# Kernel tuning notes

Hardware: AMD Instinct MI355X
Metric: run time of the kernel (lower is better)

## Reference

```python
import jax, jax.numpy as jnp
import numpy as np
import math

B, S, E = 2, 2048, 2048
H, KVH = 16, 4
HD = E // H  # 128
ROPE_BASE = 10000.0


def _rope_cos_sin(seq_len, dim, base=ROPE_BASE):
    inv_freq = 1.0 / (base ** (jnp.arange(0, dim, 2, dtype=jnp.float32) / dim))
    t = jnp.arange(seq_len, dtype=jnp.float32)
    freqs = jnp.outer(t, inv_freq)            # [S, dim/2]
    emb = jnp.concatenate([freqs, freqs], -1)  # [S, dim]
    return jnp.cos(emb), jnp.sin(emb)          # each [S, dim]


def _rotate_half(x):
    h = x.shape[-1] // 2
    return jnp.concatenate([-x[..., h:], x[..., :h]], axis=-1)


def setup_inputs() -> dict:
    key = jax.random.key(0)
    ks = jax.random.split(key, 6)
    x = jax.random.normal(ks[0], (B, S, E), dtype=jnp.float32)
    # xavier_uniform for Linear(in, out): weight stored as [out, in] in torch;
    # we store transposed [in, out] for x @ W.
    def xavier(k, fan_in, fan_out):
        a = math.sqrt(6.0 / (fan_in + fan_out))
        return jax.random.uniform(k, (fan_in, fan_out), jnp.float32, -a, a)
    wq = xavier(ks[1], E, H * HD)
    wk = xavier(ks[2], E, KVH * HD)
    wv = xavier(ks[3], E, KVH * HD)
    wo = xavier(ks[4], E, E)
    # causal mask: True above diagonal => masked
    attn_mask = jnp.triu(jnp.ones((S, S), dtype=bool), k=1)
    return {"x": x, "wq": wq, "wk": wk, "wv": wv, "wo": wo, "attn_mask": attn_mask}


def reference(x, wq, wk, wv, wo, attn_mask):
    b, s, _ = x.shape
    q = (x @ wq).reshape(b, s, H, HD).transpose(0, 2, 1, 3)     # [B,H,S,HD]
    k = (x @ wk).reshape(b, s, KVH, HD).transpose(0, 2, 1, 3)   # [B,KVH,S,HD]
    v = (x @ wv).reshape(b, s, KVH, HD).transpose(0, 2, 1, 3)
    cos, sin = _rope_cos_sin(s, HD)
    cos = cos[None, None]  # [1,1,S,HD]
    sin = sin[None, None]
    q = q * cos + _rotate_half(q) * sin
    k = k * cos + _rotate_half(k) * sin
    # repeat KV heads to match Q heads (GQA)
    groups = H // KVH
    k = jnp.repeat(k, groups, axis=1)  # [B,H,S,HD]
    v = jnp.repeat(v, groups, axis=1)
    scale = 1.0 / math.sqrt(HD)
    scores = jnp.einsum('bhqd,bhkd->bhqk', q, k) * scale  # [B,H,S,S]
    scores = jnp.where(attn_mask[None, None], -jnp.inf, scores)
    attn = jax.nn.softmax(scores, axis=-1)
    out = jnp.einsum('bhqk,bhkd->bhqd', attn, v)  # [B,H,S,HD]
    out = out.transpose(0, 2, 1, 3).reshape(b, s, E)
    return out @ wo
```

## Files before the change

### kernel.cpp

```cpp
#include <hip/hip_runtime.h>
#include <math.h>

#define S_LEN 2048
#define EDIM  2048
#define HDIM  128

typedef __attribute__((ext_vector_type(8))) __bf16 bf16x8;
typedef __attribute__((ext_vector_type(4))) __bf16 bf16x4;
typedef __attribute__((ext_vector_type(4))) float  f32x4;

__device__ __forceinline__ f32x4 mfma16x16x32(bf16x8 a, bf16x8 b, f32x4 c) {
  return __builtin_amdgcn_mfma_f32_16x16x32_bf16(a, b, c, 0, 0, 0);
}

__device__ __forceinline__ void gload_lds16(const __bf16* g, __bf16* l) {
  __builtin_amdgcn_global_load_lds(
      (const __attribute__((address_space(1))) void*)g,
      (__attribute__((address_space(3))) void*)l, 16, 0, 0);
}

__global__ void zero_flag(int* f) { *f = 0; }

__global__ void probe_dtype(const unsigned int* __restrict__ x, int* __restrict__ flag) {
  const int tid = threadIdx.x;
  int cnt = 0;
  for (int i = tid; i < 4096; i += 256) {
    unsigned e = (x[i] >> 7) & 0xFFu;
    cnt += (e >= 110u && e <= 135u) ? 1 : 0;
  }
  #pragma unroll
  for (int m = 1; m < 64; m <<= 1) cnt += __shfl_xor(cnt, m, 64);
  if ((tid & 63) == 0) atomicAdd(flag, cnt);
}

__global__ __launch_bounds__(256) void xconv(const void* __restrict__ xv,
                                             __bf16* __restrict__ xb,
                                             const int* __restrict__ flag) {
  const bool bf = (*flag > 2048);
  const size_t base = ((size_t)blockIdx.x * 256 + threadIdx.x) * 8;
  bf16x8 v;
  if (bf) {
    v = *(const bf16x8*)((const __bf16*)xv + base);
  } else {
    const float* xf = (const float*)xv + base;
    float4 f0 = *(const float4*)(xf);
    float4 f1 = *(const float4*)(xf + 4);
    v[0] = (__bf16)f0.x; v[1] = (__bf16)f0.y; v[2] = (__bf16)f0.z; v[3] = (__bf16)f0.w;
    v[4] = (__bf16)f1.x; v[5] = (__bf16)f1.y; v[6] = (__bf16)f1.z; v[7] = (__bf16)f1.w;
  }
  *(bf16x8*)(xb + base) = v;
}

__global__ __launch_bounds__(256) void trans_w(const void* __restrict__ Wv,
                                               __bf16* __restrict__ WT,
                                               int Kd, int Nd,
                                               const int* __restrict__ flag) {
  const bool bf = (*flag > 2048);
  __shared__ __bf16 t[64 * 72];
  const int tid = threadIdx.x;
  const int n0 = blockIdx.x * 64, k0 = blockIdx.y * 64;
  #pragma unroll
  for (int it = 0; it < 2; ++it) {
    int q = tid + it * 256;
    int r = q >> 3, c8 = q & 7;
    size_t gb = (size_t)(k0 + r) * Nd + n0 + c8 * 8;
    bf16x8 v;
    if (bf) {
      v = *(const bf16x8*)((const __bf16*)Wv + gb);
    } else {
      const float* wf = (const float*)Wv + gb;
      float4 f0 = *(const float4*)(wf);
      float4 f1 = *(const float4*)(wf + 4);
      v[0] = (__bf16)f0.x; v[1] = (__bf16)f0.y; v[2] = (__bf16)f0.z; v[3] = (__bf16)f0.w;
      v[4] = (__bf16)f1.x; v[5] = (__bf16)f1.y; v[6] = (__bf16)f1.z; v[7] = (__bf16)f1.w;
    }
    int eo = (c8 * 8) ^ (((r >> 3) & 7) * 8);
    *(bf16x8*)&t[r * 72 + eo] = v;
  }
  __syncthreads();
  #pragma unroll
  for (int it = 0; it < 2; ++it) {
    int q = tid + it * 256;
    int nl = q >> 3, kc = q & 7;
    bf16x8 o;
    #pragma unroll
    for (int i = 0; i < 8; ++i)
      o[i] = t[(kc * 8 + i) * 72 + (nl ^ (kc * 8))];
    *(bf16x8*)(WT + (size_t)(n0 + nl) * Kd + k0 + kc * 8) = o;
  }
}

__global__ __launch_bounds__(256) void trans_v(const __bf16* __restrict__ SRC,
                                               __bf16* __restrict__ VT,
                                               int str, int off) {
  __shared__ __bf16 t[64 * 72];
  const int tid = threadIdx.x;
  const int n0 = blockIdx.x * 64, k0 = blockIdx.y * 64;
  #pragma unroll
  for (int it = 0; it < 2; ++it) {
    int q = tid + it * 256;
    int r = q >> 3, c8 = q & 7;
    bf16x8 v = *(const bf16x8*)(SRC + (size_t)(k0 + r) * str + off + n0 + c8 * 8);
    int eo = (c8 * 8) ^ (((r >> 3) & 7) * 8);
    *(bf16x8*)&t[r * 72 + eo] = v;
  }
  __syncthreads();
  #pragma unroll
  for (int it = 0; it < 2; ++it) {
    int q = tid + it * 256;
    int nl = q >> 3, kc = q & 7;
    bf16x8 o;
    #pragma unroll
    for (int i = 0; i < 8; ++i)
      o[i] = t[(kc * 8 + i) * 72 + (nl ^ (kc * 8))];
    *(bf16x8*)(VT + (size_t)(n0 + nl) * 4096 + k0 + kc * 8) = o;
  }
}

__global__ __launch_bounds__(256) void gemm_tt(
    const __bf16* __restrict__ A, const __bf16* __restrict__ BT,
    void* __restrict__ Cv, int M, int N, int Kd,
    const int* __restrict__ flag, int cForceBf)
{
  const bool cbf = cForceBf || (*flag > 2048);
  __shared__ __bf16 sa[128 * 64];
  __shared__ __bf16 sb[128 * 64];
  const int tid = threadIdx.x;
  const int lane = tid & 63, w = tid >> 6;
  const int l15 = lane & 15, lg = lane >> 4;
  const int wr = w >> 1, wc = w & 1;
  const int m0 = blockIdx.y * 128, n0 = blockIdx.x * 128;
  const int lrow = lane >> 3, lcol = (lane & 7) * 8;

  f32x4 acc[4][4];
  #pragma unroll
  for (int i = 0; i < 4; ++i)
    #pragma unroll
    for (int j = 0; j < 4; ++j) acc[i][j] = (f32x4)(0.f);

  const __bf16* Ab = A + (size_t)(m0 + w * 32 + lrow) * Kd + lcol;
  const __bf16* Bb = BT + (size_t)(n0 + w * 32 + lrow) * Kd + lcol;

  for (int k0 = 0; k0 < Kd; k0 += 64) {
    __syncthreads();
    #pragma unroll
    for (int c = 0; c < 4; ++c) {
      gload_lds16(Ab + (size_t)(8 * c) * Kd + k0, &sa[(w * 4 + c) * 512]);
      gload_lds16(Bb + (size_t)(8 * c) * Kd + k0, &sb[(w * 4 + c) * 512]);
    }
    __syncthreads();
    #pragma unroll
    for (int ks = 0; ks < 2; ++ks) {
      bf16x8 af[4], bfr[4];
      #pragma unroll
      for (int i = 0; i < 4; ++i)
        af[i] = *(const bf16x8*)&sa[(wr * 64 + i * 16 + l15) * 64 + ks * 32 + lg * 8];
      #pragma unroll
      for (int j = 0; j < 4; ++j)
        bfr[j] = *(const bf16x8*)&sb[(wc * 64 + j * 16 + l15) * 64 + ks * 32 + lg * 8];
      #pragma unroll
      for (int i = 0; i < 4; ++i)
        #pragma unroll
        for (int j = 0; j < 4; ++j)
          acc[i][j] = mfma16x16x32(af[i], bfr[j], acc[i][j]);
    }
  }
  __bf16* Cb = (__bf16*)Cv;
  float*  Cf = (float*)Cv;
  #pragma unroll
  for (int i = 0; i < 4; ++i)
    #pragma unroll
    for (int j = 0; j < 4; ++j)
      #pragma unroll
      for (int r = 0; r < 4; ++r) {
        int row = m0 + wr * 64 + i * 16 + lg * 4 + r;
        int col = n0 + wc * 64 + j * 16 + l15;
        if (cbf) Cb[(size_t)row * N + col] = (__bf16)acc[i][j][r];
        else     Cf[(size_t)row * N + col] = acc[i][j][r];
      }
}

__global__ __launch_bounds__(256) void rope_bf16(__bf16* __restrict__ buf, int lognh,
                                                 int strideElems, float scale)
{
  const int idx = blockIdx.x * 256 + threadIdx.x;
  const int g   = idx & 7;
  const int h   = (idx >> 3) & ((1 << lognh) - 1);
  const int row = idx >> (3 + lognh);
  const int t   = row & (S_LEN - 1);
  __bf16* p = buf + (size_t)row * strideElems + h * HDIM + g * 8;
  bf16x8 v0 = *(bf16x8*)(p);
  bf16x8 v1 = *(bf16x8*)(p + 64);
  bf16x8 o0, o1;
  #pragma unroll
  for (int j = 0; j < 8; ++j) {
    int i = g * 8 + j;
    float inv = exp2f(-(float)i * 0.2076205059304601f);
    float ang = (float)t * inv;
    float sn, cs;
    sincosf(ang, &sn, &cs);
    cs *= scale; sn *= scale;
    float x0 = (float)v0[j], x1 = (float)v1[j];
    o0[j] = (__bf16)(x0 * cs - x1 * sn);
    o1[j] = (__bf16)(x1 * cs + x0 * sn);
  }
  *(bf16x8*)(p)      = o0;
  *(bf16x8*)(p + 64) = o1;
}

__device__ __forceinline__ void sm_fixed(
    f32x4 (&st)[4], float& l,
    __bf16* pls, int l15, int lg, int qglob, int kv0, bool diag,
    bf16x8& pa0, bf16x8& pa1)
{
  float rs = 0.f;
  #pragma unroll
  for (int kt = 0; kt < 4; ++kt) {
    bf16x4 pk;
    #pragma unroll
    for (int r = 0; r < 4; ++r) {
      float s = st[kt][r] - 16.f;
      if (diag && (kv0 + kt * 16 + lg * 4 + r > qglob)) s = -1e30f;
      float e = exp2f(s);
      rs += e;
      pk[r] = (__bf16)e;
    }
    *(bf16x4*)&pls[l15 * 72 + kt * 16 + lg * 4] = pk;
  }
  rs += __shfl_xor(rs, 16, 64);
  rs += __shfl_xor(rs, 32, 64);
  l += rs;
  pa0 = *(const bf16x8*)&pls[l15 * 72 + lg * 8];
  pa1 = *(const bf16x8*)&pls[l15 * 72 + 32 + lg * 8];
}

__global__ __launch_bounds__(256, 4) void flash_fwd(
    const __bf16* __restrict__ Q, const __bf16* __restrict__ Km,
    const __bf16* __restrict__ VT, __bf16* __restrict__ O, int qkstr)
{
  __shared__ __bf16 ks[2 * 64 * 128];
  __shared__ __bf16 vt[2 * 64 * 128];
  __shared__ __bf16 pl[4][16 * 72];
  const int id = blockIdx.x;
  const int c8b = id & 255, k = id >> 8;
  const int bh = c8b & 31, g = c8b >> 5;
  const int t = (k == 0) ? g : (k == 1) ? (15 - g) : (k == 2) ? (16 + g) : (31 - g);
  const int b  = bh >> 4, h = bh & 15;
  const int kvh = h >> 2;
  const int tid = threadIdx.x;
  const int lane = tid & 63, w = tid >> 6;
  const int l15 = lane & 15, lg = lane >> 4;
  const int q0 = t * 64 + w * 16;
  const int rbase = tid >> 4, colc = tid & 15;
  const int vd = tid >> 3, vkc = tid & 7;

  const __bf16* kgb = Km + (size_t)(b * S_LEN) * qkstr + kvh * HDIM + colc * 8;
  const __bf16* vgb = VT + (size_t)(kvh * HDIM + vd) * (2 * S_LEN) + b * S_LEN + vkc * 8;

  bf16x8 aq[4];
  {
    const __bf16* qa = Q + (size_t)(b * S_LEN + q0 + l15) * qkstr + h * HDIM + lg * 8;
    #pragma unroll
    for (int c = 0; c < 4; ++c) aq[c] = *(const bf16x8*)(qa + c * 32);
  }
  f32x4 o[8];
  float l = 0.f;
  #pragma unroll
  for (int c = 0; c < 8; ++c) o[c] = (f32x4)(0.f);

  const int rswz = ((l15 & 7) << 4) ^ (((l15 >> 3) & 1) << 6);

  bf16x8 kreg[4], vreg[4];
  #pragma unroll
  for (int it = 0; it < 4; ++it) {
    kreg[it] = *(const bf16x8*)(kgb + (size_t)(rbase + it * 16) * qkstr);
    vreg[it] = *(const bf16x8*)(vgb + (size_t)(it * 32) * (2 * S_LEN));
  }

  for (int j = 0; j <= t; ++j) {
    const int kv0 = j * 64;
    const int cur = (j & 1) * 16384;
    #pragma unroll
    for (int it = 0; it < 4; ++it) {
      int krow = rbase + it * 16;
      int kbyt = ((krow * 256 + colc * 16) ^ (((krow & 7) << 4) ^ (((krow >> 3) & 1) << 6))) + cur;
      *(bf16x8*)((char*)ks + kbyt) = kreg[it];
      int vrow = vd + it * 32;
      int vbyt = ((vrow * 128 + vkc * 16) ^ ((vrow & 7) << 4)) + cur;
      *(bf16x8*)((char*)vt + vbyt) = vreg[it];
    }
    __syncthreads();
    if (j < t) {
      #pragma unroll
      for (int it = 0; it < 4; ++it) {
        kreg[it] = *(const bf16x8*)(kgb + (size_t)(kv0 + 64 + rbase + it * 16) * qkstr);
        vreg[it] = *(const bf16x8*)(vgb + (size_t)(it * 32) * (2 * S_LEN) + kv0 + 64);
      }
    }

    f32x4 st[4];
    __builtin_amdgcn_s_setprio(1);
    #pragma unroll
    for (int kt = 0; kt < 4; ++kt) {
      st[kt] = (f32x4)(0.f);
      #pragma unroll
      for (int c = 0; c < 4; ++c) {
        int byt = (((kt * 16 + l15) * 256 + c * 64 + lg * 16) ^ rswz) + cur;
        bf16x8 kf = *(const bf16x8*)((const char*)ks + byt);
        st[kt] = mfma16x16x32(kf, aq[c], st[kt]);
      }
    }
    __builtin_amdgcn_s_setprio(0);

    bf16x8 pa0, pa1;
    sm_fixed(st, l, &pl[w][0], l15, lg, q0 + l15, kv0, j == t, pa0, pa1);

    __builtin_amdgcn_s_setprio(1);
    #pragma unroll
    for (int c = 0; c < 8; ++c) {
      int d0 = c * 16 + l15;
      int byt0 = ((d0 * 128 + lg * 16) ^ ((d0 & 7) << 4)) + cur;
      int byt1 = ((d0 * 128 + lg * 16 + 64) ^ ((d0 & 7) << 4)) + cur;
      bf16x8 bv0 = *(const bf16x8*)((const char*)vt + byt0);
      bf16x8 bv1 = *(const bf16x8*)((const char*)vt + byt1);
      o[c] = mfma16x16x32(pa0, bv0, o[c]);
      o[c] = mfma16x16x32(pa1, bv1, o[c]);
    }
    __builtin_amdgcn_s_setprio(0);
  }

  float lo[4];
  #pragma unroll
  for (int r = 0; r < 4; ++r) lo[r] = __shfl(l, lg * 4 + r, 64);
  #pragma unroll
  for (int c = 0; c < 8; ++c)
    #pragma unroll
    for (int r = 0; r < 4; ++r)
      O[(size_t)(b * S_LEN + q0 + lg * 4 + r) * EDIM + h * HDIM + c * 16 + l15] =
          (__bf16)(o[c][r] / lo[r]);
}

extern "C" void kernel_launch(void* const* d_in, const int* in_sizes, int n_in,
                              void* d_out, int out_size, void* d_ws, size_t ws_size,
                              hipStream_t stream) {
  const void* x  = d_in[0];
  const void* wq = d_in[1];
  const void* wk = d_in[2];
  const void* wv = d_in[3];
  const void* wo = d_in[4];
  char* ws = (char*)d_ws;
  int*    flagp = (int*)ws;
  __bf16* QKVw = (__bf16*)(ws + 1024);
  __bf16* R4   = (__bf16*)(ws + 1024 + (24u << 20));
  __bf16* R5   = (__bf16*)(ws + 1024 + (40u << 20));
  __bf16* VwT  = R5 + (size_t)2048 * 2048;
  const float QSCALE = 1.4426950408889634f * 0.08838834764831845f;
  dim3 blk(256);
  zero_flag<<<1, 1, 0, stream>>>(flagp);
  probe_dtype<<<1, blk, 0, stream>>>((const unsigned int*)x, flagp);
  xconv<<<4096, blk, 0, stream>>>(x, R4, flagp);

  trans_w<<<dim3(32, 32), blk, 0, stream>>>(wq, R5, EDIM, EDIM, flagp);
  trans_w<<<dim3(8, 32),  blk, 0, stream>>>(wk, R5 + (size_t)2048 * 2048, EDIM, 512, flagp);
  trans_w<<<dim3(8, 32),  blk, 0, stream>>>(wv, R5 + (size_t)2560 * 2048, EDIM, 512, flagp);
  gemm_tt<<<dim3(24, 32), blk, 0, stream>>>(R4, R5, QKVw, 4096, 3072, 2048, flagp, 1);

  rope_bf16<<<2048, blk, 0, stream>>>(QKVw, 4, 3072, QSCALE);
  rope_bf16<<<512,  blk, 0, stream>>>(QKVw + 2048, 2, 3072, 1.0f);
  trans_v<<<dim3(8, 64), blk, 0, stream>>>(QKVw, VwT, 3072, 2560);

  trans_w<<<dim3(32, 32), blk, 0, stream>>>(wo, R5, EDIM, EDIM, flagp);
  flash_fwd<<<dim3(1024), blk, 0, stream>>>(QKVw, QKVw + 2048, VwT, R4, 3072);
  gemm_tt<<<dim3(16, 32), blk, 0, stream>>>(R4, R5, d_out, 4096, 2048, 2048, flagp, 0);
}
```

Baseline: 265.8 us.

## Fold flag zeroing into probe, skip xconv copy for bf16, shrink GEMM K-tile

Removes the separate zero_flag launch by zeroing the flag inside probe_dtype. In the bf16-input path, xconv now returns early and the QKV GEMM reads the raw input directly instead of a copy. The GEMM K-tile drops from 64 to 32, which halves LDS use per block (possibly raising occupancy) but doubles the number of barrier-synchronized iterations. With the default fp32 inputs only the tile change and the saved launch matter.

```diff
diff --git a/kernel.cpp b/kernel.cpp
--- a/kernel.cpp
+++ b/kernel.cpp
@@ -19,10 +19,10 @@
       (__attribute__((address_space(3))) void*)l, 16, 0, 0);
 }
 
-__global__ void zero_flag(int* f) { *f = 0; }
-
 __global__ void probe_dtype(const unsigned int* __restrict__ x, int* __restrict__ flag) {
   const int tid = threadIdx.x;
+  if (tid == 0) *flag = 0;
+  __syncthreads();
   int cnt = 0;
   for (int i = tid; i < 4096; i += 256) {
     unsigned e = (x[i] >> 7) & 0xFFu;
@@ -36,18 +36,14 @@
 __global__ __launch_bounds__(256) void xconv(const void* __restrict__ xv,
                                              __bf16* __restrict__ xb,
                                              const int* __restrict__ flag) {
-  const bool bf = (*flag > 2048);
+  if (*flag > 2048) return;
   const size_t base = ((size_t)blockIdx.x * 256 + threadIdx.x) * 8;
+  const float* xf = (const float*)xv + base;
+  float4 f0 = *(const float4*)(xf);
+  float4 f1 = *(const float4*)(xf + 4);
   bf16x8 v;
-  if (bf) {
-    v = *(const bf16x8*)((const __bf16*)xv + base);
-  } else {
-    const float* xf = (const float*)xv + base;
-    float4 f0 = *(const float4*)(xf);
-    float4 f1 = *(const float4*)(xf + 4);
-    v[0] = (__bf16)f0.x; v[1] = (__bf16)f0.y; v[2] = (__bf16)f0.z; v[3] = (__bf16)f0.w;
-    v[4] = (__bf16)f1.x; v[5] = (__bf16)f1.y; v[6] = (__bf16)f1.z; v[7] = (__bf16)f1.w;
-  }
+  v[0] = (__bf16)f0.x; v[1] = (__bf16)f0.y; v[2] = (__bf16)f0.z; v[3] = (__bf16)f0.w;
+  v[4] = (__bf16)f1.x; v[5] = (__bf16)f1.y; v[6] = (__bf16)f1.z; v[7] = (__bf16)f1.w;
   *(bf16x8*)(xb + base) = v;
 }
 
@@ -100,7 +96,7 @@
   for (int it = 0; it < 2; ++it) {
     int q = tid + it * 256;
     int r = q >> 3, c8 = q & 7;
-    bf16x8 v = *(const bf16x8*)(SRC + (size_t)(k0 + r) * str + off + n0 + c8 * 8);
+    bf16x8 v = *(const bf16x8*)(SRC + (size_t)(k0 + r) * str + off + c8 * 8 + n0);
     int eo = (c8 * 8) ^ (((r >> 3) & 7) * 8);
     *(bf16x8*)&t[r * 72 + eo] = v;
   }
@@ -118,19 +114,22 @@
 }
 
 __global__ __launch_bounds__(256) void gemm_tt(
-    const __bf16* __restrict__ A, const __bf16* __restrict__ BT,
+    const __bf16* __restrict__ A, const void* __restrict__ Araw,
+    const __bf16* __restrict__ BT,
     void* __restrict__ Cv, int M, int N, int Kd,
     const int* __restrict__ flag, int cForceBf)
 {
-  const bool cbf = cForceBf || (*flag > 2048);
-  __shared__ __bf16 sa[128 * 64];
-  __shared__ __bf16 sb[128 * 64];
+  const bool inBf = (*flag > 2048);
+  const bool cbf = cForceBf || inBf;
+  const __bf16* Ause = inBf ? (const __bf16*)Araw : A;
+  __shared__ __bf16 sa[128 * 32];
+  __shared__ __bf16 sb[128 * 32];
   const int tid = threadIdx.x;
   const int lane = tid & 63, w = tid >> 6;
   const int l15 = lane & 15, lg = lane >> 4;
   const int wr = w >> 1, wc = w & 1;
   const int m0 = blockIdx.y * 128, n0 = blockIdx.x * 128;
-  const int lrow = lane >> 3, lcol = (lane & 7) * 8;
+  const int lrow = lane >> 2, lcol = (lane & 3) * 8;
 
   f32x4 acc[4][4];
   #pragma unroll
@@ -138,32 +137,29 @@
     #pragma unroll
     for (int j = 0; j < 4; ++j) acc[i][j] = (f32x4)(0.f);
 
-  const __bf16* Ab = A + (size_t)(m0 + w * 32 + lrow) * Kd + lcol;
-  const __bf16* Bb = BT + (size_t)(n0 + w * 32 + lrow) * Kd + lcol;
-
-  for (int k0 = 0; k0 < Kd; k0 += 64) {
+  const __bf16* Ab = Ause + (size_t)(m0 + w * 32 + lrow) * Kd + lcol;
+  const __bf16* Bb = BT   + (size_t)(n0 + w * 32 + lrow) * Kd + lcol;
+
+  for (int k0 = 0; k0 < Kd; k0 += 32) {
     __syncthreads();
     #pragma unroll
-    for (int c = 0; c < 4; ++c) {
-      gload_lds16(Ab + (size_t)(8 * c) * Kd + k0, &sa[(w * 4 + c) * 512]);
-      gload_lds16(Bb + (size_t)(8 * c) * Kd + k0, &sb[(w * 4 + c) * 512]);
+    for (int c = 0; c < 2; ++c) {
+      gload_lds16(Ab + (size_t)(16 * c) * Kd + k0, &sa[(w * 2 + c) * 512]);
+      gload_lds16(Bb + (size_t)(16 * c) * Kd + k0, &sb[(w * 2 + c) * 512]);
     }
     __syncthreads();
-    #pragma unroll
-    for (int ks = 0; ks < 2; ++ks) {
-      bf16x8 af[4], bfr[4];
-      #pragma unroll
-      for (int i = 0; i < 4; ++i)
-        af[i] = *(const bf16x8*)&sa[(wr * 64 + i * 16 + l15) * 64 + ks * 32 + lg * 8];
+    bf16x8 af[4], bfr[4];
+    #pragma unroll
+    for (int i = 0; i < 4; ++i)
+      af[i] = *(const bf16x8*)&sa[(wr * 64 + i * 16 + l15) * 32 + lg * 8];
+    #pragma unroll
+    for (int j = 0; j < 4; ++j)
+      bfr[j] = *(const bf16x8*)&sb[(wc * 64 + j * 16 + l15) * 32 + lg * 8];
+    #pragma unroll
+    for (int i = 0; i < 4; ++i)
       #pragma unroll
       for (int j = 0; j < 4; ++j)
-        bfr[j] = *(const bf16x8*)&sb[(wc * 64 + j * 16 + l15) * 64 + ks * 32 + lg * 8];
-      #pragma unroll
-      for (int i = 0; i < 4; ++i)
-        #pragma unroll
-        for (int j = 0; j < 4; ++j)
-          acc[i][j] = mfma16x16x32(af[i], bfr[j], acc[i][j]);
-    }
+        acc[i][j] = mfma16x16x32(af[i], bfr[j], acc[i][j]);
   }
   __bf16* Cb = (__bf16*)Cv;
   float*  Cf = (float*)Cv;
@@ -354,16 +350,16 @@
   __bf16* R4   = (__bf16*)(ws + 1024 + (24u << 20));
   __bf16* R5   = (__bf16*)(ws + 1024 + (40u << 20));
   __bf16* VwT  = R5 + (size_t)2048 * 2048;
+
   const float QSCALE = 1.4426950408889634f * 0.08838834764831845f;
   dim3 blk(256);
-  zero_flag<<<1, 1, 0, stream>>>(flagp);
   probe_dtype<<<1, blk, 0, stream>>>((const unsigned int*)x, flagp);
   xconv<<<4096, blk, 0, stream>>>(x, R4, flagp);
 
   trans_w<<<dim3(32, 32), blk, 0, stream>>>(wq, R5, EDIM, EDIM, flagp);
   trans_w<<<dim3(8, 32),  blk, 0, stream>>>(wk, R5 + (size_t)2048 * 2048, EDIM, 512, flagp);
   trans_w<<<dim3(8, 32),  blk, 0, stream>>>(wv, R5 + (size_t)2560 * 2048, EDIM, 512, flagp);
-  gemm_tt<<<dim3(24, 32), blk, 0, stream>>>(R4, R5, QKVw, 4096, 3072, 2048, flagp, 1);
+  gemm_tt<<<dim3(24, 32), blk, 0, stream>>>(R4, x, R5, QKVw, 4096, 3072, 2048, flagp, 1);
 
   rope_bf16<<<2048, blk, 0, stream>>>(QKVw, 4, 3072, QSCALE);
   rope_bf16<<<512,  blk, 0, stream>>>(QKVw + 2048, 2, 3072, 1.0f);
@@ -371,5 +367,5 @@
 
   trans_w<<<dim3(32, 32), blk, 0, stream>>>(wo, R5, EDIM, EDIM, flagp);
   flash_fwd<<<dim3(1024), blk, 0, stream>>>(QKVw, QKVw + 2048, VwT, R4, 3072);
-  gemm_tt<<<dim3(16, 32), blk, 0, stream>>>(R4, R5, d_out, 4096, 2048, 2048, flagp, 0);
-}
+  gemm_tt<<<dim3(16, 32), blk, 0, stream>>>(R4, R4, R5, d_out, 4096, 2048, 2048, flagp, 0);
+}
```

Measured after the change: 247.0 us. -7.1%, faster.
